# Kernel tuning notes

Measured on AMD Instinct MI355X. Metric: run time of the kernel, lower is better.

## Reference

```python
import jax, jax.numpy as jnp
import numpy as np

HIDDEN = 1024
MEM = 50
MAX_POS = 200
BATCH, SEQ = 256, 200


def setup_inputs() -> dict:
    key = jax.random.key(0)
    ks = jax.random.split(key, 5)
    x = jax.random.normal(ks[0], (BATCH, SEQ, HIDDEN), dtype=jnp.float32)
    spatial_memory = jax.random.normal(ks[1], (MEM, HIDDEN), dtype=jnp.float32)
    pos_encoding = jax.random.normal(ks[2], (1, MAX_POS, HIDDEN), dtype=jnp.float32)
    # nn.Linear(2H, H): weight [H, 2H], bias [H]
    bound = 1.0 / np.sqrt(2 * HIDDEN)
    gate_w = jax.random.uniform(ks[3], (HIDDEN, 2 * HIDDEN), jnp.float32, -bound, bound)
    gate_b = jax.random.uniform(ks[4], (HIDDEN,), jnp.float32, -bound, bound)
    return {"x": x, "spatial_memory": spatial_memory, "pos_encoding": pos_encoding,
            "gate_w": gate_w, "gate_b": gate_b}


def reference(x, spatial_memory, pos_encoding, gate_w, gate_b):
    seq_len = x.shape[1]
    # add position encoding (sliced to seq_len)
    feats = x + pos_encoding[:, :seq_len, :]                      # [B,S,H]
    # cross-attention over small fixed memory bank
    sim = jnp.einsum('bsh,mh->bsm', feats, spatial_memory)        # [B,S,M]
    w = jax.nn.softmax(sim, axis=-1)
    mem_read = jnp.einsum('bsm,mh->bsh', w, spatial_memory)       # [B,S,H]
    # gated update: sigmoid(Linear(concat)) -- split weight to avoid concat
    w_f, w_m = gate_w[:, :HIDDEN], gate_w[:, HIDDEN:]
    gate = jax.nn.sigmoid(jnp.einsum('bsh,oh->bso', feats, w_f)
                          + jnp.einsum('bsh,oh->bso', mem_read, w_m)
                          + gate_b)
    return feats + gate * mem_read
```

## Files before the change

### kernel.cpp

```cpp
#include <hip/hip_runtime.h>
#include <cstdint>
#include <cstddef>

#define HD   1024
#define SEQL 200
#define MEMN 50
#define RTOT 51200
#define PK   72

typedef float  f4    __attribute__((ext_vector_type(4)));
typedef float  f32x4 __attribute__((ext_vector_type(4)));
typedef short  s16x8 __attribute__((ext_vector_type(8)));
typedef unsigned short u16;
typedef unsigned short u16x4 __attribute__((ext_vector_type(4)));
typedef unsigned short u16x8 __attribute__((ext_vector_type(8)));

__device__ __forceinline__ u16 f2bf(float f) {
    unsigned u = __builtin_bit_cast(unsigned, f);
    u += 0x7FFFu + ((u >> 16) & 1u);
    return (u16)(u >> 16);
}
__device__ __forceinline__ float bf2f(u16 h) {
    unsigned u = ((unsigned)h) << 16;
    return __builtin_bit_cast(float, u);
}

#define GLOAD_LDS16(g, l) __builtin_amdgcn_global_load_lds( \
    (const __attribute__((address_space(1))) unsigned int*)(g), \
    (__attribute__((address_space(3))) unsigned int*)(l), 16, 0, 0)

#define WAITV3 asm volatile("s_waitcnt vmcnt(3)" ::: "memory")
#define WAITV0 asm volatile("s_waitcnt vmcnt(0)" ::: "memory")
#define LGKMFENCE asm volatile("s_waitcnt lgkmcnt(0)" ::: "memory")
#define SCHB   __builtin_amdgcn_sched_barrier(0)

__global__ __launch_bounds__(256) void k_cvt_w(const float* __restrict__ gw,
                                               u16* __restrict__ gwB)
{
    const size_t i = ((size_t)blockIdx.x * 256 + threadIdx.x) * 8;
    f4 v0 = *(const f4*)&gw[i];
    f4 v1 = *(const f4*)&gw[i + 4];
    u16x4 b0 = { f2bf(v0.x), f2bf(v0.y), f2bf(v0.z), f2bf(v0.w) };
    u16x4 b1 = { f2bf(v1.x), f2bf(v1.y), f2bf(v1.z), f2bf(v1.w) };
    *(u16x4*)&gwB[i]     = b0;
    *(u16x4*)&gwB[i + 4] = b1;
}

__global__ __launch_bounds__(256) void k_prep_mem(const float* __restrict__ sm,
                                                  u16* __restrict__ memHi,
                                                  u16* __restrict__ memT,
                                                  u16* __restrict__ memSH,
                                                  u16* __restrict__ memSL)
{
    const int idx = blockIdx.x * 256 + threadIdx.x;
    const int m  = idx >> 8;
    const int h0 = (idx & 255) * 4;
    f4 v = {0.f, 0.f, 0.f, 0.f};
    if (m < MEMN) v = *(const f4*)&sm[(size_t)m * HD + h0];
    u16x4 hi = { f2bf(v.x), f2bf(v.y), f2bf(v.z), f2bf(v.w) };
    f4 hv = { bf2f(hi.x), bf2f(hi.y), bf2f(hi.z), bf2f(hi.w) };
    f4 lv = v - hv;
    u16x4 lo = { f2bf(lv.x), f2bf(lv.y), f2bf(lv.z), f2bf(lv.w) };
    *(u16x4*)&memHi[(size_t)m * HD + h0] = hi;
    memT[(size_t)(h0 + 0) * 64 + m] = hi.x;
    memT[(size_t)(h0 + 1) * 64 + m] = hi.y;
    memT[(size_t)(h0 + 2) * 64 + m] = hi.z;
    memT[(size_t)(h0 + 3) * 64 + m] = hi.w;
    const int p = h0 >> 6, s = (h0 >> 3) & 7, e = h0 & 7;
    const size_t sw = (size_t)p * 4096 + m * 64 + ((s ^ (m & 7)) << 3) + e;
    *(u16x4*)&memSH[sw] = hi;
    *(u16x4*)&memSL[sw] = lo;
}

__global__ __launch_bounds__(256) void k_mwm(const u16* __restrict__ memHi,
                                             const u16* __restrict__ gwB,
                                             u16* __restrict__ MWmT)
{
    const int tid = threadIdx.x, lane = tid & 63, w = tid >> 6;
    const int fr = lane & 15, fk = (lane >> 4) * 8, jr = (lane >> 4) * 4;
    const int ob = blockIdx.x * 64 + w * 16;
    f32x4 acc[4] = {};
    for (int ks = 0; ks < 32; ++ks) {
        s16x8 b = *(const s16x8*)&gwB[(size_t)(ob + fr) * 2048 + 1024 + ks * 32 + fk];
        #pragma unroll
        for (int mt = 0; mt < 4; ++mt) {
            s16x8 a = *(const s16x8*)&memHi[(size_t)(mt * 16 + fr) * HD + ks * 32 + fk];
            acc[mt] = __builtin_amdgcn_mfma_f32_16x16x32_bf16(a, b, acc[mt], 0, 0, 0);
        }
    }
    #pragma unroll
    for (int mt = 0; mt < 4; ++mt)
        #pragma unroll
        for (int j = 0; j < 4; ++j)
            MWmT[(size_t)(ob + fr) * 64 + mt * 16 + jr + j] = f2bf(acc[mt][j]);
}

__global__ __launch_bounds__(256) void k_pre(
    const float* __restrict__ x, const float* __restrict__ pos,
    const u16* __restrict__ memSH, const u16* __restrict__ memSL,
    u16* __restrict__ featsB, u16* __restrict__ wBg)
{
    __shared__ u16 fHi[64 * PK];
    __shared__ u16 fLo[64 * PK];
    __shared__ u16 memH[2][64 * 64];
    __shared__ u16 memL[2][64 * 64];

    const int tid  = threadIdx.x;
    const int r0   = blockIdx.x * 64;
    const int lane = tid & 63, w = tid >> 6;
    const int fr   = lane & 15, sg = lane >> 4;
    const int fk   = sg * 8, jr = sg * 4;

    const int srow = tid >> 2;
    const int scol = (tid & 3) * 16;
    const int prow = (r0 + srow) % SEQL;
    const float* xrow = &x[(size_t)(r0 + srow) * HD];
    const float* prp  = &pos[(size_t)prow * HD];

    f4 xa[4], pa[4];
    #pragma unroll
    for (int i = 0; i < 4; ++i) {
        xa[i] = *(const f4*)&xrow[scol + i * 4];
        pa[i] = *(const f4*)&prp[scol + i * 4];
    }
    GLOAD_LDS16(memSH + tid * 8,        &memH[0][tid * 8]);
    GLOAD_LDS16(memSH + 2048 + tid * 8, &memH[0][2048 + tid * 8]);
    GLOAD_LDS16(memSL + tid * 8,        &memL[0][tid * 8]);
    GLOAD_LDS16(memSL + 2048 + tid * 8, &memL[0][2048 + tid * 8]);

    f32x4 acc[4] = {};

    for (int p = 0; p < 16; ++p) {
        const int b = p & 1;
        WAITV0;

        {
            f4 f0 = xa[0] + pa[0], f1 = xa[1] + pa[1];
            f4 f2 = xa[2] + pa[2], f3 = xa[3] + pa[3];
            u16x8 h0 = { f2bf(f0.x), f2bf(f0.y), f2bf(f0.z), f2bf(f0.w),
                         f2bf(f1.x), f2bf(f1.y), f2bf(f1.z), f2bf(f1.w) };
            u16x8 h1 = { f2bf(f2.x), f2bf(f2.y), f2bf(f2.z), f2bf(f2.w),
                         f2bf(f3.x), f2bf(f3.y), f2bf(f3.z), f2bf(f3.w) };
            *(u16x8*)&featsB[(size_t)(r0 + srow) * HD + p * 64 + scol]     = h0;
            *(u16x8*)&featsB[(size_t)(r0 + srow) * HD + p * 64 + scol + 8] = h1;
            f4 hv0 = { bf2f(h0[0]), bf2f(h0[1]), bf2f(h0[2]), bf2f(h0[3]) };
            f4 hv1 = { bf2f(h0[4]), bf2f(h0[5]), bf2f(h0[6]), bf2f(h0[7]) };
            f4 hv2 = { bf2f(h1[0]), bf2f(h1[1]), bf2f(h1[2]), bf2f(h1[3]) };
            f4 hv3 = { bf2f(h1[4]), bf2f(h1[5]), bf2f(h1[6]), bf2f(h1[7]) };
            f4 l0 = f0 - hv0, l1 = f1 - hv1, l2 = f2 - hv2, l3 = f3 - hv3;
            u16x8 lo0 = { f2bf(l0.x), f2bf(l0.y), f2bf(l0.z), f2bf(l0.w),
                          f2bf(l1.x), f2bf(l1.y), f2bf(l1.z), f2bf(l1.w) };
            u16x8 lo1 = { f2bf(l2.x), f2bf(l2.y), f2bf(l2.z), f2bf(l2.w),
                          f2bf(l3.x), f2bf(l3.y), f2bf(l3.z), f2bf(l3.w) };
            *(u16x8*)&fHi[srow * PK + scol]     = h0;
            *(u16x8*)&fHi[srow * PK + scol + 8] = h1;
            *(u16x8*)&fLo[srow * PK + scol]     = lo0;
            *(u16x8*)&fLo[srow * PK + scol + 8] = lo1;
        }
        LGKMFENCE;
        __builtin_amdgcn_s_barrier();

        if (p < 15) {
            const size_t mo = (size_t)(p + 1) * 4096;
            GLOAD_LDS16(memSH + mo + tid * 8,        &memH[b ^ 1][tid * 8]);
            GLOAD_LDS16(memSH + mo + 2048 + tid * 8, &memH[b ^ 1][2048 + tid * 8]);
            GLOAD_LDS16(memSL + mo + tid * 8,        &memL[b ^ 1][tid * 8]);
            GLOAD_LDS16(memSL + mo + 2048 + tid * 8, &memL[b ^ 1][2048 + tid * 8]);
            const int c = (p + 1) * 64 + scol;
            #pragma unroll
            for (int i = 0; i < 4; ++i) {
                xa[i] = *(const f4*)&xrow[c + i * 4];
                pa[i] = *(const f4*)&prp[c + i * 4];
            }
        }

        #pragma unroll
        for (int ks = 0; ks < 2; ++ks) {
            s16x8 aH = *(const s16x8*)&fHi[(16 * w + fr) * PK + ks * 32 + fk];
            s16x8 aL = *(const s16x8*)&fLo[(16 * w + fr) * PK + ks * 32 + fk];
            #pragma unroll
            for (int n = 0; n < 4; ++n) {
                const int m = n * 16 + fr;
                const int slot = ((ks * 4 + sg) ^ (m & 7)) * 8;
                s16x8 bH = *(const s16x8*)&memH[b][m * 64 + slot];
                s16x8 bL = *(const s16x8*)&memL[b][m * 64 + slot];
                acc[n] = __builtin_amdgcn_mfma_f32_16x16x32_bf16(aH, bH, acc[n], 0, 0, 0);
                acc[n] = __builtin_amdgcn_mfma_f32_16x16x32_bf16(aH, bL, acc[n], 0, 0, 0);
                acc[n] = __builtin_amdgcn_mfma_f32_16x16x32_bf16(aL, bH, acc[n], 0, 0, 0);
            }
        }
    }

    #pragma unroll
    for (int j = 0; j < 4; ++j) {
        const int rg = r0 + 16 * w + jr + j;
        float v[4];
        float mx = -1e30f;
        #pragma unroll
        for (int n = 0; n < 4; ++n) {
            v[n] = acc[n][j];
            const int m = n * 16 + fr;
            if (m < MEMN) mx = fmaxf(mx, v[n]);
        }
        #pragma unroll
        for (int d = 1; d < 16; d <<= 1) mx = fmaxf(mx, __shfl_xor(mx, d));
        float e[4], s = 0.f;
        #pragma unroll
        for (int n = 0; n < 4; ++n) {
            const int m = n * 16 + fr;
            e[n] = (m < MEMN) ? __expf(v[n] - mx) : 0.f;
            s += e[n];
        }
        #pragma unroll
        for (int d = 1; d < 16; d <<= 1) s += __shfl_xor(s, d);
        const float inv = 1.f / s;
        #pragma unroll
        for (int n = 0; n < 4; ++n)
            wBg[(size_t)rg * 64 + n * 16 + fr] = f2bf(e[n] * inv);
    }
}

__global__ __launch_bounds__(512) void k_gate_out(
    const u16* __restrict__ featsB, const u16* __restrict__ wBg,
    const u16* __restrict__ gwB, const u16* __restrict__ memT,
    const u16* __restrict__ MWmT, const float* __restrict__ gb,
    float* __restrict__ out)
{
    __shared__ u16 As[2][256 * 32];
    __shared__ u16 Bs[2][128 * 32];

    const int tid = threadIdx.x;
    int bid = blockIdx.x;
    bid = (bid & 7) * 200 + (bid >> 3);
    const int mt = bid >> 3, nt = bid & 7;
    const int row0 = mt * 256, col0 = nt * 128;
    const int lane = tid & 63, wave = tid >> 6;
    const int wm = wave >> 1, wn = wave & 1;
    const int fr = lane & 15, fk = (lane >> 4) * 8;

    f32x4 acc[4][4] = {};

    const int sr = tid >> 2;
    const int sc = (tid & 3) * 8;

    auto stage = [&](int buf, int kt) {
        if (kt < 32) {
            const int k0 = kt * 32;
            GLOAD_LDS16(featsB + (size_t)(row0 + sr) * HD + k0 + sc,       &As[buf][tid * 8]);
            GLOAD_LDS16(featsB + (size_t)(row0 + 128 + sr) * HD + k0 + sc, &As[buf][4096 + tid * 8]);
            GLOAD_LDS16(gwB + (size_t)(col0 + sr) * 2048 + k0 + sc,        &Bs[buf][tid * 8]);
        } else {
            const int k0 = (kt - 32) * 32;
            GLOAD_LDS16(wBg + (size_t)(row0 + sr) * 64 + k0 + sc,          &As[buf][tid * 8]);
            GLOAD_LDS16(wBg + (size_t)(row0 + 128 + sr) * 64 + k0 + sc,    &As[buf][4096 + tid * 8]);
            GLOAD_LDS16(MWmT + (size_t)(col0 + sr) * 64 + k0 + sc,         &Bs[buf][tid * 8]);
        }
    };

    stage(0, 0);
    int cur = 0;

    for (int kt = 0; kt < 34; ++kt) {
        if (kt < 33) {
            stage(cur ^ 1, kt + 1);
            WAITV3;
        } else {
            WAITV0;
        }
        __builtin_amdgcn_s_barrier();
        SCHB;

        s16x8 aF[4], bF[4];
        #pragma unroll
        for (int m = 0; m < 4; ++m)
            aF[m] = *(const s16x8*)&As[cur][(wm * 64 + m * 16 + fr) * 32 + fk];
        #pragma unroll
        for (int n = 0; n < 4; ++n)
            bF[n] = *(const s16x8*)&Bs[cur][(wn * 64 + n * 16 + fr) * 32 + fk];
        #pragma unroll
        for (int m = 0; m < 4; ++m)
            #pragma unroll
            for (int n = 0; n < 4; ++n)
                acc[m][n] = __builtin_amdgcn_mfma_f32_16x16x32_bf16(
                    aF[m], bF[n], acc[m][n], 0, 0, 0);

        SCHB;
        __builtin_amdgcn_s_barrier();
        cur ^= 1;
    }

    #pragma unroll
    for (int m = 0; m < 4; ++m) {
        const size_t ab = (size_t)(row0 + wm * 64 + m * 16 + fr) * 64 + fk;
        s16x8 a2_0 = *(const s16x8*)&wBg[ab];
        s16x8 a2_1 = *(const s16x8*)&wBg[ab + 32];
        #pragma unroll
        for (int n = 0; n < 4; ++n) {
            const size_t cb = (size_t)(col0 + wn * 64 + n * 16 + fr) * 64 + fk;
            s16x8 bT0 = *(const s16x8*)&memT[cb];
            s16x8 bT1 = *(const s16x8*)&memT[cb + 32];
            f32x4 accR = {};
            accR = __builtin_amdgcn_mfma_f32_16x16x32_bf16(a2_0, bT0, accR, 0, 0, 0);
            accR = __builtin_amdgcn_mfma_f32_16x16x32_bf16(a2_1, bT1, accR, 0, 0, 0);

            const int crow = row0 + wm * 64 + m * 16 + (lane >> 4) * 4;
            const int ccol = col0 + wn * 64 + n * 16 + fr;
            const float bias = gb[ccol];
            #pragma unroll
            for (int j = 0; j < 4; ++j) {
                const size_t idx = (size_t)(crow + j) * HD + ccol;
                const float fe = bf2f(featsB[idx]);
                const float pre = acc[m][n][j] + bias;
                const float g = 1.0f / (1.0f + __expf(-pre));
                out[idx] = fe + g * accR[j];
            }
        }
    }
}

extern "C" void kernel_launch(void* const* d_in, const int* in_sizes, int n_in,
                              void* d_out, int out_size, void* d_ws, size_t ws_size,
                              hipStream_t stream)
{
    const float* x   = (const float*)d_in[0];
    const float* sm  = (const float*)d_in[1];
    const float* pos = (const float*)d_in[2];
    const float* gw  = (const float*)d_in[3];
    const float* gb  = (const float*)d_in[4];
    float* out = (float*)d_out;

    u16* featsB = (u16*)d_ws;
    u16* gwB    = featsB + (size_t)RTOT * HD;
    u16* wBg    = gwB + (size_t)HD * 2048;
    u16* memHi  = wBg + (size_t)RTOT * 64;
    u16* memT   = memHi + 64 * HD;
    u16* MWmT   = memT + (size_t)HD * 64;
    u16* memSH  = MWmT + (size_t)HD * 64;
    u16* memSL  = memSH + (size_t)64 * HD;

    k_cvt_w<<<dim3(1024), dim3(256), 0, stream>>>(gw, gwB);
    k_prep_mem<<<dim3(64), dim3(256), 0, stream>>>(sm, memHi, memT, memSH, memSL);
    k_mwm<<<dim3(16), dim3(256), 0, stream>>>(memHi, gwB, MWmT);
    k_pre<<<dim3(RTOT / 64), dim3(256), 0, stream>>>(x, pos, memSH, memSL,
                                                     featsB, wBg);
    k_gate_out<<<dim3(1600), dim3(512), 0, stream>>>(featsB, wBg, gwB, memT,
                                                     MWmT, gb, out);
}
```

Baseline: 370.0 us.

## Run feats·W_f gate GEMM in FP8 with swizzled LDS tiles

The main gate GEMM (feats times the feats half of the gate weight) now uses FP8 operands and the 16x16x32 fp8 MFMA instead of bf16. The weight is prescaled by 64 and the result rescaled afterwards. k_pre and k_cvt_w emit extra FP8 copies of feats and the weight. The small wBg·MWmT term is moved out of the main K loop into the epilogue, which halves the bytes staged per K step and shortens the loop. LDS tiles use an XOR swizzle to avoid bank conflicts. The cost is an extra FP8 write of feats in the pre-pass and reduced precision in the gate pre-activation, which may hurt accuracy.

Result: slower. 533.6 us (+44.2%).

```diff
diff --git a/kernel.cpp b/kernel.cpp
--- a/kernel.cpp
+++ b/kernel.cpp
@@ -12,6 +12,10 @@
 typedef float  f32x4 __attribute__((ext_vector_type(4)));
 typedef short  s16x8 __attribute__((ext_vector_type(8)));
 typedef unsigned short u16;
+typedef unsigned char  u8;
+typedef unsigned int   u32;
+typedef unsigned int   u32x2 __attribute__((ext_vector_type(2)));
+typedef unsigned int   u32x4 __attribute__((ext_vector_type(4)));
 typedef unsigned short u16x4 __attribute__((ext_vector_type(4)));
 typedef unsigned short u16x8 __attribute__((ext_vector_type(8)));
 
@@ -35,7 +39,8 @@
 #define SCHB   __builtin_amdgcn_sched_barrier(0)
 
 __global__ __launch_bounds__(256) void k_cvt_w(const float* __restrict__ gw,
-                                               u16* __restrict__ gwB)
+                                               u16* __restrict__ gwB,
+                                               u8* __restrict__ gwF8)
 {
     const size_t i = ((size_t)blockIdx.x * 256 + threadIdx.x) * 8;
     f4 v0 = *(const f4*)&gw[i];
@@ -44,6 +49,17 @@
     u16x4 b1 = { f2bf(v1.x), f2bf(v1.y), f2bf(v1.z), f2bf(v1.w) };
     *(u16x4*)&gwB[i]     = b0;
     *(u16x4*)&gwB[i + 4] = b1;
+
+    const int k = (int)(i & 2047);
+    if (k < 1024) {
+        f4 s0 = v0 * 64.0f, s1 = v1 * 64.0f;
+        u32 q0 = __builtin_amdgcn_cvt_pk_fp8_f32(s0.x, s0.y, 0, false);
+        q0     = __builtin_amdgcn_cvt_pk_fp8_f32(s0.z, s0.w, q0, true);
+        u32 q1 = __builtin_amdgcn_cvt_pk_fp8_f32(s1.x, s1.y, 0, false);
+        q1     = __builtin_amdgcn_cvt_pk_fp8_f32(s1.z, s1.w, q1, true);
+        u32x2 qv = { q0, q1 };
+        *(u32x2*)&gwF8[(i >> 11) * 1024 + k] = qv;
+    }
 }
 
 __global__ __launch_bounds__(256) void k_prep_mem(const float* __restrict__ sm,
@@ -98,7 +114,8 @@
 __global__ __launch_bounds__(256) void k_pre(
     const float* __restrict__ x, const float* __restrict__ pos,
     const u16* __restrict__ memSH, const u16* __restrict__ memSL,
-    u16* __restrict__ featsB, u16* __restrict__ wBg)
+    u16* __restrict__ featsB, u8* __restrict__ featsF8,
+    u16* __restrict__ wBg)
 {
     __shared__ u16 fHi[64 * PK];
     __shared__ u16 fLo[64 * PK];
@@ -143,6 +160,17 @@
                          f2bf(f3.x), f2bf(f3.y), f2bf(f3.z), f2bf(f3.w) };
             *(u16x8*)&featsB[(size_t)(r0 + srow) * HD + p * 64 + scol]     = h0;
             *(u16x8*)&featsB[(size_t)(r0 + srow) * HD + p * 64 + scol + 8] = h1;
+            u32 q0 = __builtin_amdgcn_cvt_pk_fp8_f32(f0.x, f0.y, 0, false);
+            q0     = __builtin_amdgcn_cvt_pk_fp8_f32(f0.z, f0.w, q0, true);
+            u32 q1 = __builtin_amdgcn_cvt_pk_fp8_f32(f1.x, f1.y, 0, false);
+            q1     = __builtin_amdgcn_cvt_pk_fp8_f32(f1.z, f1.w, q1, true);
+            u32 q2 = __builtin_amdgcn_cvt_pk_fp8_f32(f2.x, f2.y, 0, false);
+            q2     = __builtin_amdgcn_cvt_pk_fp8_f32(f2.z, f2.w, q2, true);
+            u32 q3 = __builtin_amdgcn_cvt_pk_fp8_f32(f3.x, f3.y, 0, false);
+            q3     = __builtin_amdgcn_cvt_pk_fp8_f32(f3.z, f3.w, q3, true);
+            u32x4 qv = { q0, q1, q2, q3 };
+            *(u32x4*)&featsF8[(size_t)(r0 + srow) * HD + p * 64 + scol] = qv;
+
             f4 hv0 = { bf2f(h0[0]), bf2f(h0[1]), bf2f(h0[2]), bf2f(h0[3]) };
             f4 hv1 = { bf2f(h0[4]), bf2f(h0[5]), bf2f(h0[6]), bf2f(h0[7]) };
             f4 hv2 = { bf2f(h1[0]), bf2f(h1[1]), bf2f(h1[2]), bf2f(h1[3]) };
@@ -221,13 +249,13 @@
 }
 
 __global__ __launch_bounds__(512) void k_gate_out(
-    const u16* __restrict__ featsB, const u16* __restrict__ wBg,
-    const u16* __restrict__ gwB, const u16* __restrict__ memT,
-    const u16* __restrict__ MWmT, const float* __restrict__ gb,
-    float* __restrict__ out)
-{
-    __shared__ u16 As[2][256 * 32];
-    __shared__ u16 Bs[2][128 * 32];
+    const u16* __restrict__ featsB, const u8* __restrict__ featsF8,
+    const u16* __restrict__ wBg, const u8* __restrict__ gwF8,
+    const u16* __restrict__ memT, const u16* __restrict__ MWmT,
+    const float* __restrict__ gb, float* __restrict__ out)
+{
+    __shared__ u8 As[2][256 * 64];
+    __shared__ u8 Bs[2][128 * 64];
 
     const int tid = threadIdx.x;
     int bid = blockIdx.x;
@@ -236,32 +264,37 @@
     const int row0 = mt * 256, col0 = nt * 128;
     const int lane = tid & 63, wave = tid >> 6;
     const int wm = wave >> 1, wn = wave & 1;
-    const int fr = lane & 15, fk = (lane >> 4) * 8;
+    const int fr = lane & 15, sg = lane >> 4;
 
     f32x4 acc[4][4] = {};
 
     const int sr = tid >> 2;
-    const int sc = (tid & 3) * 8;
+    const int sq = tid & 3;
 
     auto stage = [&](int buf, int kt) {
-        if (kt < 32) {
-            const int k0 = kt * 32;
-            GLOAD_LDS16(featsB + (size_t)(row0 + sr) * HD + k0 + sc,       &As[buf][tid * 8]);
-            GLOAD_LDS16(featsB + (size_t)(row0 + 128 + sr) * HD + k0 + sc, &As[buf][4096 + tid * 8]);
-            GLOAD_LDS16(gwB + (size_t)(col0 + sr) * 2048 + k0 + sc,        &Bs[buf][tid * 8]);
-        } else {
-            const int k0 = (kt - 32) * 32;
-            GLOAD_LDS16(wBg + (size_t)(row0 + sr) * 64 + k0 + sc,          &As[buf][tid * 8]);
-            GLOAD_LDS16(wBg + (size_t)(row0 + 128 + sr) * 64 + k0 + sc,    &As[buf][4096 + tid * 8]);
-            GLOAD_LDS16(MWmT + (size_t)(col0 + sr) * 64 + k0 + sc,         &Bs[buf][tid * 8]);
+        const int k0 = kt * 64;
+        {
+            const int r = sr;
+            GLOAD_LDS16(featsF8 + (size_t)(row0 + r) * HD + k0 + ((sq ^ (r & 3)) * 16),
+                        &As[buf][r * 64 + sq * 16]);
+        }
+        {
+            const int r = 128 + sr;
+            GLOAD_LDS16(featsF8 + (size_t)(row0 + r) * HD + k0 + ((sq ^ (r & 3)) * 16),
+                        &As[buf][r * 64 + sq * 16]);
+        }
+        {
+            const int r = sr;
+            GLOAD_LDS16(gwF8 + (size_t)(col0 + r) * HD + k0 + ((sq ^ (r & 3)) * 16),
+                        &Bs[buf][r * 64 + sq * 16]);
         }
     };
 
     stage(0, 0);
     int cur = 0;
 
-    for (int kt = 0; kt < 34; ++kt) {
-        if (kt < 33) {
+    for (int kt = 0; kt < 16; ++kt) {
+        if (kt < 15) {
             stage(cur ^ 1, kt + 1);
             WAITV3;
         } else {
@@ -270,19 +303,28 @@
         __builtin_amdgcn_s_barrier();
         SCHB;
 
-        s16x8 aF[4], bF[4];
-        #pragma unroll
-        for (int m = 0; m < 4; ++m)
-            aF[m] = *(const s16x8*)&As[cur][(wm * 64 + m * 16 + fr) * 32 + fk];
-        #pragma unroll
-        for (int n = 0; n < 4; ++n)
-            bF[n] = *(const s16x8*)&Bs[cur][(wn * 64 + n * 16 + fr) * 32 + fk];
-        #pragma unroll
-        for (int m = 0; m < 4; ++m)
-            #pragma unroll
-            for (int n = 0; n < 4; ++n)
-                acc[m][n] = __builtin_amdgcn_mfma_f32_16x16x32_bf16(
-                    aF[m], bF[n], acc[m][n], 0, 0, 0);
+        #pragma unroll
+        for (int ks = 0; ks < 2; ++ks) {
+            long aF[4], bF[4];
+            #pragma unroll
+            for (int m = 0; m < 4; ++m) {
+                const int r = wm * 64 + m * 16 + fr;
+                const int q = (ks * 2 + (sg >> 1)) ^ (r & 3);
+                aF[m] = *(const long*)&As[cur][r * 64 + q * 16 + (sg & 1) * 8];
+            }
+            #pragma unroll
+            for (int n = 0; n < 4; ++n) {
+                const int r = wn * 64 + n * 16 + fr;
+                const int q = (ks * 2 + (sg >> 1)) ^ (r & 3);
+                bF[n] = *(const long*)&Bs[cur][r * 64 + q * 16 + (sg & 1) * 8];
+            }
+            #pragma unroll
+            for (int m = 0; m < 4; ++m)
+                #pragma unroll
+                for (int n = 0; n < 4; ++n)
+                    acc[m][n] = __builtin_amdgcn_mfma_f32_16x16x32_fp8_fp8(
+                        aF[m], bF[n], acc[m][n], 0, 0, 0);
+        }
 
         SCHB;
         __builtin_amdgcn_s_barrier();
@@ -291,26 +333,31 @@
 
     #pragma unroll
     for (int m = 0; m < 4; ++m) {
-        const size_t ab = (size_t)(row0 + wm * 64 + m * 16 + fr) * 64 + fk;
+        const size_t ab = (size_t)(row0 + wm * 64 + m * 16 + fr) * 64 + sg * 8;
         s16x8 a2_0 = *(const s16x8*)&wBg[ab];
         s16x8 a2_1 = *(const s16x8*)&wBg[ab + 32];
         #pragma unroll
         for (int n = 0; n < 4; ++n) {
-            const size_t cb = (size_t)(col0 + wn * 64 + n * 16 + fr) * 64 + fk;
+            const size_t cb = (size_t)(col0 + wn * 64 + n * 16 + fr) * 64 + sg * 8;
+            s16x8 bW0 = *(const s16x8*)&MWmT[cb];
+            s16x8 bW1 = *(const s16x8*)&MWmT[cb + 32];
             s16x8 bT0 = *(const s16x8*)&memT[cb];
             s16x8 bT1 = *(const s16x8*)&memT[cb + 32];
+            f32x4 accT = {};
+            accT = __builtin_amdgcn_mfma_f32_16x16x32_bf16(a2_0, bW0, accT, 0, 0, 0);
+            accT = __builtin_amdgcn_mfma_f32_16x16x32_bf16(a2_1, bW1, accT, 0, 0, 0);
             f32x4 accR = {};
             accR = __builtin_amdgcn_mfma_f32_16x16x32_bf16(a2_0, bT0, accR, 0, 0, 0);
             accR = __builtin_amdgcn_mfma_f32_16x16x32_bf16(a2_1, bT1, accR, 0, 0, 0);
 
-            const int crow = row0 + wm * 64 + m * 16 + (lane >> 4) * 4;
+            const int crow = row0 + wm * 64 + m * 16 + sg * 4;
             const int ccol = col0 + wn * 64 + n * 16 + fr;
             const float bias = gb[ccol];
             #pragma unroll
             for (int j = 0; j < 4; ++j) {
                 const size_t idx = (size_t)(crow + j) * HD + ccol;
                 const float fe = bf2f(featsB[idx]);
-                const float pre = acc[m][n][j] + bias;
+                const float pre = acc[m][n][j] * 0.015625f + accT[j] + bias;
                 const float g = 1.0f / (1.0f + __expf(-pre));
                 out[idx] = fe + g * accR[j];
             }
@@ -337,12 +384,14 @@
     u16* MWmT   = memT + (size_t)HD * 64;
     u16* memSH  = MWmT + (size_t)HD * 64;
     u16* memSL  = memSH + (size_t)64 * HD;
-
-    k_cvt_w<<<dim3(1024), dim3(256), 0, stream>>>(gw, gwB);
+    u8*  featsF8 = (u8*)(memSL + (size_t)64 * HD);
+    u8*  gwF8    = featsF8 + (size_t)RTOT * HD;
+
+    k_cvt_w<<<dim3(1024), dim3(256), 0, stream>>>(gw, gwB, gwF8);
     k_prep_mem<<<dim3(64), dim3(256), 0, stream>>>(sm, memHi, memT, memSH, memSL);
     k_mwm<<<dim3(16), dim3(256), 0, stream>>>(memHi, gwB, MWmT);
     k_pre<<<dim3(RTOT / 64), dim3(256), 0, stream>>>(x, pos, memSH, memSL,
-                                                     featsB, wBg);
-    k_gate_out<<<dim3(1600), dim3(512), 0, stream>>>(featsB, wBg, gwB, memT,
-                                                     MWmT, gb, out);
-}
+                                                     featsB, featsF8, wBg);
+    k_gate_out<<<dim3(1600), dim3(512), 0, stream>>>(featsB, featsF8, wBg, gwF8,
+                                                     memT, MWmT, gb, out);
+}
```

## Repack gate weights into MFMA fragment order and load B directly to registers

Applied to the files above, without the earlier changes.

Adds a repack kernel that lays the bf16 gate weights and MW product out in per-wave MFMA fragment order. The main GEMM then loads B operands straight from global memory into registers, double-buffered one k-step ahead, instead of staging them through LDS. LDS traffic and LDS footprint drop for the B side. In exchange, each wave fetches its own B fragments from global/L2 with no sharing across waves in the block, and there is an extra small launch and workspace buffer. The vmcnt wait threshold is raised so outstanding register loads don't force an early wait.

New measurement: 420.0 us. +13.5%, slower.

```diff
diff --git a/kernel.cpp b/kernel.cpp
--- a/kernel.cpp
+++ b/kernel.cpp
@@ -29,7 +29,7 @@
     (const __attribute__((address_space(1))) unsigned int*)(g), \
     (__attribute__((address_space(3))) unsigned int*)(l), 16, 0, 0)
 
-#define WAITV3 asm volatile("s_waitcnt vmcnt(3)" ::: "memory")
+#define WAITV6 asm volatile("s_waitcnt vmcnt(6)" ::: "memory")
 #define WAITV0 asm volatile("s_waitcnt vmcnt(0)" ::: "memory")
 #define LGKMFENCE asm volatile("s_waitcnt lgkmcnt(0)" ::: "memory")
 #define SCHB   __builtin_amdgcn_sched_barrier(0)
@@ -93,6 +93,28 @@
         #pragma unroll
         for (int j = 0; j < 4; ++j)
             MWmT[(size_t)(ob + fr) * 64 + mt * 16 + jr + j] = f2bf(acc[mt][j]);
+}
+
+__global__ __launch_bounds__(256) void k_repack(const u16* __restrict__ gwB,
+                                                const u16* __restrict__ MWmT,
+                                                u16* __restrict__ gwFrag)
+{
+    const int tid = threadIdx.x;
+    const int chunk = blockIdx.x * 4 + (tid >> 6);
+    const int lane = tid & 63;
+    const int fr = lane & 15, sg = lane >> 4;
+    const int kt = chunk % 34;
+    const int c2 = chunk / 34;
+    const int n   = c2 & 3;
+    const int wnn = (c2 >> 2) & 1;
+    const int nt  = c2 >> 3;
+    const int row = nt * 128 + wnn * 64 + n * 16 + fr;
+    s16x8 v;
+    if (kt < 32)
+        v = *(const s16x8*)&gwB[(size_t)row * 2048 + kt * 32 + sg * 8];
+    else
+        v = *(const s16x8*)&MWmT[(size_t)row * 64 + (kt - 32) * 32 + sg * 8];
+    *(s16x8*)&gwFrag[(size_t)chunk * 512 + lane * 8] = v;
 }
 
 __global__ __launch_bounds__(256) void k_pre(
@@ -222,12 +244,10 @@
 
 __global__ __launch_bounds__(512) void k_gate_out(
     const u16* __restrict__ featsB, const u16* __restrict__ wBg,
-    const u16* __restrict__ gwB, const u16* __restrict__ memT,
-    const u16* __restrict__ MWmT, const float* __restrict__ gb,
-    float* __restrict__ out)
+    const u16* __restrict__ gwFrag, const u16* __restrict__ memT,
+    const float* __restrict__ gb, float* __restrict__ out)
 {
     __shared__ u16 As[2][256 * 32];
-    __shared__ u16 Bs[2][128 * 32];
 
     const int tid = threadIdx.x;
     int bid = blockIdx.x;
@@ -243,51 +263,62 @@
     const int sr = tid >> 2;
     const int sc = (tid & 3) * 8;
 
-    auto stage = [&](int buf, int kt) {
+    auto stageA = [&](int buf, int kt) {
         if (kt < 32) {
             const int k0 = kt * 32;
             GLOAD_LDS16(featsB + (size_t)(row0 + sr) * HD + k0 + sc,       &As[buf][tid * 8]);
             GLOAD_LDS16(featsB + (size_t)(row0 + 128 + sr) * HD + k0 + sc, &As[buf][4096 + tid * 8]);
-            GLOAD_LDS16(gwB + (size_t)(col0 + sr) * 2048 + k0 + sc,        &Bs[buf][tid * 8]);
         } else {
             const int k0 = (kt - 32) * 32;
             GLOAD_LDS16(wBg + (size_t)(row0 + sr) * 64 + k0 + sc,          &As[buf][tid * 8]);
             GLOAD_LDS16(wBg + (size_t)(row0 + 128 + sr) * 64 + k0 + sc,    &As[buf][4096 + tid * 8]);
-            GLOAD_LDS16(MWmT + (size_t)(col0 + sr) * 64 + k0 + sc,         &Bs[buf][tid * 8]);
         }
     };
 
-    stage(0, 0);
-    int cur = 0;
-
-    for (int kt = 0; kt < 34; ++kt) {
-        if (kt < 33) {
-            stage(cur ^ 1, kt + 1);
-            WAITV3;
+    const u16* bbase = gwFrag + (size_t)((nt * 2 + wn) * 4) * 34 * 512 + lane * 8;
+
+    s16x8 bA[4], bB[4];
+    #define LOADB(dst, kt)                                                 \
+        { _Pragma("unroll")                                                \
+          for (int n_ = 0; n_ < 4; ++n_)                                   \
+              dst[n_] = *(const s16x8*)(bbase + ((size_t)n_ * 34 + (kt)) * 512); }
+
+    #define STEP(buf, kt, breg, last)                                      \
+        {                                                                  \
+            if (!(last)) { stageA((buf) ^ 1, (kt) + 1); }                  \
+            if (!(last)) { WAITV6; } else { WAITV0; }                      \
+            __builtin_amdgcn_s_barrier();                                  \
+            SCHB;                                                          \
+            s16x8 aF[4];                                                   \
+            _Pragma("unroll")                                              \
+            for (int m_ = 0; m_ < 4; ++m_)                                 \
+                aF[m_] = *(const s16x8*)&As[buf][(wm * 64 + m_ * 16 + fr) * 32 + fk]; \
+            _Pragma("unroll")                                              \
+            for (int m_ = 0; m_ < 4; ++m_)                                 \
+                _Pragma("unroll")                                          \
+                for (int n_ = 0; n_ < 4; ++n_)                             \
+                    acc[m_][n_] = __builtin_amdgcn_mfma_f32_16x16x32_bf16( \
+                        aF[m_], breg[n_], acc[m_][n_], 0, 0, 0);           \
+            SCHB;                                                          \
+            __builtin_amdgcn_s_barrier();                                  \
+        }
+
+    stageA(0, 0);
+    LOADB(bA, 0);
+
+    for (int it = 0; it < 17; ++it) {
+        const int k0 = it * 2;
+        LOADB(bB, k0 + 1);
+        STEP(0, k0, bA, false);
+        if (it < 16) {
+            LOADB(bA, k0 + 2);
+            STEP(1, k0 + 1, bB, false);
         } else {
-            WAITV0;
-        }
-        __builtin_amdgcn_s_barrier();
-        SCHB;
-
-        s16x8 aF[4], bF[4];
-        #pragma unroll
-        for (int m = 0; m < 4; ++m)
-            aF[m] = *(const s16x8*)&As[cur][(wm * 64 + m * 16 + fr) * 32 + fk];
-        #pragma unroll
-        for (int n = 0; n < 4; ++n)
-            bF[n] = *(const s16x8*)&Bs[cur][(wn * 64 + n * 16 + fr) * 32 + fk];
-        #pragma unroll
-        for (int m = 0; m < 4; ++m)
-            #pragma unroll
-            for (int n = 0; n < 4; ++n)
-                acc[m][n] = __builtin_amdgcn_mfma_f32_16x16x32_bf16(
-                    aF[m], bF[n], acc[m][n], 0, 0, 0);
-
-        SCHB;
-        __builtin_amdgcn_s_barrier();
-        cur ^= 1;
-    }
+            STEP(1, 33, bB, true);
+        }
+    }
+    #undef STEP
+    #undef LOADB
 
     #pragma unroll
     for (int m = 0; m < 4; ++m) {
@@ -337,12 +368,14 @@
     u16* MWmT   = memT + (size_t)HD * 64;
     u16* memSH  = MWmT + (size_t)HD * 64;
     u16* memSL  = memSH + (size_t)64 * HD;
+    u16* gwFrag = memSL + (size_t)64 * HD;
 
     k_cvt_w<<<dim3(1024), dim3(256), 0, stream>>>(gw, gwB);
     k_prep_mem<<<dim3(64), dim3(256), 0, stream>>>(sm, memHi, memT, memSH, memSL);
     k_mwm<<<dim3(16), dim3(256), 0, stream>>>(memHi, gwB, MWmT);
+    k_repack<<<dim3(544), dim3(256), 0, stream>>>(gwB, MWmT, gwFrag);
     k_pre<<<dim3(RTOT / 64), dim3(256), 0, stream>>>(x, pos, memSH, memSL,
                                                      featsB, wBg);
-    k_gate_out<<<dim3(1600), dim3(512), 0, stream>>>(featsB, wBg, gwB, memT,
-                                                     MWmT, gb, out);
-}
+    k_gate_out<<<dim3(1600), dim3(512), 0, stream>>>(featsB, wBg, gwFrag,
+                                                     memT, gb, out);
+}
```

## Enlarge gate GEMM tile to 256x256 with register-staged swizzled LDS pipeline

Applied to the files above, without the earlier changes.

Doubles the output tile of the gate GEMM to 256x256 with a 64-wide K step. Global loads now go through registers into XOR-swizzled LDS instead of direct global-to-LDS copies, and the loop is split into four interleaved phases with MFMA priority raised. The goal is more operand reuse per byte loaded, fewer LDS bank conflicts, and better overlap of loads with MFMA work. In exchange it uses a larger accumulator array (8x4 per wave) and about 128KB of LDS per block, which adds register pressure, limits occupancy, and makes the hand-written wait counts fragile.

New measurement: 371.7 us. About the same (+0.4%).

```diff
diff --git a/kernel.cpp b/kernel.cpp
--- a/kernel.cpp
+++ b/kernel.cpp
@@ -29,7 +29,8 @@
     (const __attribute__((address_space(1))) unsigned int*)(g), \
     (__attribute__((address_space(3))) unsigned int*)(l), 16, 0, 0)
 
-#define WAITV3 asm volatile("s_waitcnt vmcnt(3)" ::: "memory")
+#define WAITV4 asm volatile("s_waitcnt vmcnt(4)" ::: "memory")
+#define WAITV2 asm volatile("s_waitcnt vmcnt(2)" ::: "memory")
 #define WAITV0 asm volatile("s_waitcnt vmcnt(0)" ::: "memory")
 #define LGKMFENCE asm volatile("s_waitcnt lgkmcnt(0)" ::: "memory")
 #define SCHB   __builtin_amdgcn_sched_barrier(0)
@@ -220,78 +221,116 @@
     }
 }
 
-__global__ __launch_bounds__(512) void k_gate_out(
+__global__ __launch_bounds__(512, 2) void k_gate_out(
     const u16* __restrict__ featsB, const u16* __restrict__ wBg,
     const u16* __restrict__ gwB, const u16* __restrict__ memT,
     const u16* __restrict__ MWmT, const float* __restrict__ gb,
     float* __restrict__ out)
 {
-    __shared__ u16 As[2][256 * 32];
-    __shared__ u16 Bs[2][128 * 32];
+    __shared__ u16 As[2][256 * 64];
+    __shared__ u16 Bs[2][256 * 64];
 
     const int tid = threadIdx.x;
     int bid = blockIdx.x;
-    bid = (bid & 7) * 200 + (bid >> 3);
-    const int mt = bid >> 3, nt = bid & 7;
-    const int row0 = mt * 256, col0 = nt * 128;
+    bid = (bid & 7) * 100 + (bid >> 3);
+    const int mt = bid >> 2, nt = bid & 3;
+    const int row0 = mt * 256, col0 = nt * 256;
     const int lane = tid & 63, wave = tid >> 6;
-    const int wm = wave >> 1, wn = wave & 1;
-    const int fr = lane & 15, fk = (lane >> 4) * 8;
-
-    f32x4 acc[4][4] = {};
-
-    const int sr = tid >> 2;
-    const int sc = (tid & 3) * 8;
-
-    auto stage = [&](int buf, int kt) {
-        if (kt < 32) {
-            const int k0 = kt * 32;
-            GLOAD_LDS16(featsB + (size_t)(row0 + sr) * HD + k0 + sc,       &As[buf][tid * 8]);
-            GLOAD_LDS16(featsB + (size_t)(row0 + 128 + sr) * HD + k0 + sc, &As[buf][4096 + tid * 8]);
-            GLOAD_LDS16(gwB + (size_t)(col0 + sr) * 2048 + k0 + sc,        &Bs[buf][tid * 8]);
-        } else {
-            const int k0 = (kt - 32) * 32;
-            GLOAD_LDS16(wBg + (size_t)(row0 + sr) * 64 + k0 + sc,          &As[buf][tid * 8]);
-            GLOAD_LDS16(wBg + (size_t)(row0 + 128 + sr) * 64 + k0 + sc,    &As[buf][4096 + tid * 8]);
-            GLOAD_LDS16(MWmT + (size_t)(col0 + sr) * 64 + k0 + sc,         &Bs[buf][tid * 8]);
+    const int wm = wave >> 2, wn = wave & 3;
+    const int fr = lane & 15, sg = lane >> 4;
+    const int fk = sg * 8;
+
+    f32x4 acc[8][4] = {};
+    s16x8 aF[4], bF[4];
+    s16x8 rA0[2], rA1[2], rB0[2], rB1[2];
+
+    const int srow = tid >> 1;
+
+    auto loadU = [&](int kt, int unit, s16x8 r[2]) {
+        const int ks = unit >> 1, kindB = unit & 1;
+        #pragma unroll
+        for (int j = 0; j < 2; ++j) {
+            const int sl = (tid & 1) * 2 + j;
+            const u16* p;
+            if (kindB)
+                p = (kt < 16)
+                  ? gwB  + (size_t)(col0 + srow) * 2048 + kt * 64 + ks * 32 + sl * 8
+                  : MWmT + (size_t)(col0 + srow) * 64 + ks * 32 + sl * 8;
+            else
+                p = (kt < 16)
+                  ? featsB + (size_t)(row0 + srow) * HD + kt * 64 + ks * 32 + sl * 8
+                  : wBg    + (size_t)(row0 + srow) * 64 + ks * 32 + sl * 8;
+            r[j] = *(const s16x8*)p;
         }
     };
-
-    stage(0, 0);
-    int cur = 0;
-
-    for (int kt = 0; kt < 34; ++kt) {
-        if (kt < 33) {
-            stage(cur ^ 1, kt + 1);
-            WAITV3;
-        } else {
-            WAITV0;
-        }
-        __builtin_amdgcn_s_barrier();
-        SCHB;
-
-        s16x8 aF[4], bF[4];
-        #pragma unroll
-        for (int m = 0; m < 4; ++m)
-            aF[m] = *(const s16x8*)&As[cur][(wm * 64 + m * 16 + fr) * 32 + fk];
-        #pragma unroll
-        for (int n = 0; n < 4; ++n)
-            bF[n] = *(const s16x8*)&Bs[cur][(wn * 64 + n * 16 + fr) * 32 + fk];
-        #pragma unroll
-        for (int m = 0; m < 4; ++m)
-            #pragma unroll
-            for (int n = 0; n < 4; ++n)
-                acc[m][n] = __builtin_amdgcn_mfma_f32_16x16x32_bf16(
-                    aF[m], bF[n], acc[m][n], 0, 0, 0);
-
-        SCHB;
-        __builtin_amdgcn_s_barrier();
-        cur ^= 1;
-    }
+    auto writeU = [&](int b_, int unit, s16x8 r[2]) {
+        const int ks = unit >> 1, kindB = unit & 1;
+        u16* base = kindB ? &Bs[b_][0] : &As[b_][0];
+        #pragma unroll
+        for (int j = 0; j < 2; ++j) {
+            const int sl = (tid & 1) * 2 + j;
+            const int slot = (ks * 4 + sl) ^ (srow & 7);
+            *(s16x8*)&base[srow * 64 + slot * 8] = r[j];
+        }
+    };
+
+    loadU(0, 0, rA0); loadU(0, 1, rB0);
+    WAITV0;
+    writeU(0, 0, rA0); writeU(0, 1, rB0);
+    loadU(0, 2, rA1); loadU(0, 3, rB1);
+    LGKMFENCE;
+    __builtin_amdgcn_s_barrier();
+
+#define PHASE(Q, KS, MSUB, RL, RW)                                          \
+    {                                                                       \
+        _Pragma("unroll")                                                   \
+        for (int i = 0; i < 4; ++i) {                                       \
+            const int r_ = wm * 128 + ((MSUB) * 4 + i) * 16 + fr;           \
+            aF[i] = *(const s16x8*)&As[buf][r_ * 64 +                       \
+                        ((((KS) * 4) + sg) ^ (r_ & 7)) * 8];                \
+        }                                                                   \
+        if ((Q) % 2 == 0) {                                                 \
+            _Pragma("unroll")                                               \
+            for (int n = 0; n < 4; ++n) {                                   \
+                const int r_ = wn * 64 + n * 16 + fr;                       \
+                bF[n] = *(const s16x8*)&Bs[buf][r_ * 64 +                   \
+                            ((((KS) * 4) + sg) ^ (r_ & 7)) * 8];            \
+            }                                                               \
+        }                                                                   \
+        if (T < 16) {                                                       \
+            loadU(T + 1, (Q), RL);                                          \
+            WAITV4;                                                         \
+        } else if ((Q) == 0) { WAITV2; }                                    \
+        else if ((Q) == 1)   { WAITV0; }                                    \
+        if (!((Q) >= 2 && T == 16))                                         \
+            writeU(((Q) >= 2) ? (buf ^ 1) : buf, ((Q) + 2) & 3, RW);        \
+        __builtin_amdgcn_s_barrier();                                       \
+        LGKMFENCE;                                                          \
+        SCHB;                                                               \
+        __builtin_amdgcn_s_setprio(1);                                      \
+        _Pragma("unroll")                                                   \
+        for (int i = 0; i < 4; ++i)                                         \
+            _Pragma("unroll")                                               \
+            for (int n = 0; n < 4; ++n)                                     \
+                acc[(MSUB) * 4 + i][n] =                                    \
+                    __builtin_amdgcn_mfma_f32_16x16x32_bf16(                \
+                        aF[i], bF[n], acc[(MSUB) * 4 + i][n], 0, 0, 0);     \
+        __builtin_amdgcn_s_setprio(0);                                      \
+        __builtin_amdgcn_s_barrier();                                       \
+    }
+
+    for (int T = 0; T < 17; ++T) {
+        const int buf = T & 1;
+        PHASE(0, 0, 0, rA0, rA1)
+        PHASE(1, 0, 1, rB0, rB1)
+        PHASE(2, 1, 0, rA1, rA0)
+        PHASE(3, 1, 1, rB1, rB0)
+    }
+#undef PHASE
 
     #pragma unroll
-    for (int m = 0; m < 4; ++m) {
-        const size_t ab = (size_t)(row0 + wm * 64 + m * 16 + fr) * 64 + fk;
+    for (int m = 0; m < 8; ++m) {
+        const size_t ab = (size_t)(row0 + wm * 128 + m * 16 + fr) * 64 + fk;
         s16x8 a2_0 = *(const s16x8*)&wBg[ab];
         s16x8 a2_1 = *(const s16x8*)&wBg[ab + 32];
         #pragma unroll
@@ -303,7 +342,7 @@
             accR = __builtin_amdgcn_mfma_f32_16x16x32_bf16(a2_0, bT0, accR, 0, 0, 0);
             accR = __builtin_amdgcn_mfma_f32_16x16x32_bf16(a2_1, bT1, accR, 0, 0, 0);
 
-            const int crow = row0 + wm * 64 + m * 16 + (lane >> 4) * 4;
+            const int crow = row0 + wm * 128 + m * 16 + sg * 4;
             const int ccol = col0 + wn * 64 + n * 16 + fr;
             const float bias = gb[ccol];
             #pragma unroll
@@ -343,6 +382,6 @@
     k_mwm<<<dim3(16), dim3(256), 0, stream>>>(memHi, gwB, MWmT);
     k_pre<<<dim3(RTOT / 64), dim3(256), 0, stream>>>(x, pos, memSH, memSL,
                                                      featsB, wBg);
-    k_gate_out<<<dim3(1600), dim3(512), 0, stream>>>(featsB, wBg, gwB, memT,
-                                                     MWmT, gb, out);
-}
+    k_gate_out<<<dim3(800), dim3(512), 0, stream>>>(featsB, wBg, gwB, memT,
+                                                    MWmT, gb, out);
+}
```
